# Kernel optimization log

Hardware: AMD Instinct MI355X
Metric: run time of the kernel (lower is better)

## Reference

```python
import jax, jax.numpy as jnp
import numpy as np

N, E, D, ED, H = 4096, 262144, 256, 64, 8
HD = D // H


def _ln(x, g, b, eps=1e-5):
    mu = jnp.mean(x, axis=-1, keepdims=True)
    var = jnp.mean((x - mu) ** 2, axis=-1, keepdims=True)
    return (x - mu) * jax.lax.rsqrt(var + eps) * g + b


def setup_inputs() -> dict:
    key = jax.random.key(0)
    ks = jax.random.split(key, 16)
    p = lambda k, s: (0.02 * jax.random.normal(k, s, dtype=jnp.float32))
    return {
        'x': jax.random.normal(ks[0], (N, D), dtype=jnp.float32),
        'edge_index': jax.random.randint(ks[1], (2, E), 0, N, dtype=jnp.int64),
        'edge_attr': jax.random.normal(ks[2], (E, ED), dtype=jnp.float32),
        'eps': jnp.zeros((), dtype=jnp.float32),  # GINEConv train_eps initial value 0
        'Wl': p(ks[3], (ED, D)), 'bl': jnp.zeros((D,), jnp.float32),
        'W1': p(ks[4], (D, D)), 'b1': jnp.zeros((D,), jnp.float32),
        'W2': p(ks[5], (D, D)), 'b2': jnp.zeros((D,), jnp.float32),
        'ln_l_g': jnp.ones((D,), jnp.float32), 'ln_l_b': jnp.zeros((D,), jnp.float32),
        'in_w': p(ks[6], (3 * D, D)), 'in_b': jnp.zeros((3 * D,), jnp.float32),
        'out_w': p(ks[7], (D, D)), 'out_b': jnp.zeros((D,), jnp.float32),
        'ln_a_g': jnp.ones((D,), jnp.float32), 'ln_a_b': jnp.zeros((D,), jnp.float32),
        'Wf1': p(ks[8], (D, 2 * D)), 'bf1': jnp.zeros((2 * D,), jnp.float32),
        'Wf2': p(ks[9], (2 * D, D)), 'bf2': jnp.zeros((D,), jnp.float32),
        'ln_f_g': jnp.ones((D,), jnp.float32), 'ln_f_b': jnp.zeros((D,), jnp.float32),
    }


def reference(x, edge_index, edge_attr, eps, Wl, bl, W1, b1, W2, b2,
              ln_l_g, ln_l_b, in_w, in_b, out_w, out_b, ln_a_g, ln_a_b,
              Wf1, bf1, Wf2, bf2, ln_f_g, ln_f_b):
    n = x.shape[0]
    src, dst = edge_index[0], edge_index[1]
    # --- GINEConv: msg = relu(x_j + lin(edge_attr)), sum-aggregate, MLP((1+eps)x + agg)
    msg = jax.nn.relu(x[src] + edge_attr @ Wl + bl)            # [E, D]
    agg = jax.ops.segment_sum(msg, dst, num_segments=n)        # [N, D]
    h = (1.0 + eps) * x + agg
    h = jax.nn.elu(h @ W1 + b1) @ W2 + b2                      # local_mlp
    x = x + jax.nn.elu(_ln(h, ln_l_g, ln_l_b))                 # local residual (dropout=eval)
    # --- MultiheadAttention (single batch of all nodes)
    qkv = x @ in_w.T + in_b                                    # [N, 3D]
    q, k, v = jnp.split(qkv, 3, axis=-1)
    q = q.reshape(n, H, HD)
    k = k.reshape(n, H, HD)
    v = v.reshape(n, H, HD)
    scores = jnp.einsum('qhd,khd->hqk', q, k) / jnp.sqrt(jnp.float32(HD))
    attn = jax.nn.softmax(scores, axis=-1)
    o = jnp.einsum('hqk,khd->qhd', attn, v).reshape(n, D)
    o = o @ out_w.T + out_b
    x = x + _ln(o, ln_a_g, ln_a_b)
    # --- FFN (exact GELU as in torch nn.GELU default)
    f = jax.nn.gelu(x @ Wf1 + bf1, approximate=False) @ Wf2 + bf2
    x = x + _ln(f, ln_f_g, ln_f_b)
    return x
```

## Files before the change

### kernel.cpp

```cpp
#include <hip/hip_runtime.h>
#include <cstddef>

#define D 256
#define H 8
#define HD 32
#define ED 64

typedef __attribute__((ext_vector_type(8))) short short8;
typedef __attribute__((ext_vector_type(4))) short short4v;
typedef __attribute__((ext_vector_type(4))) float floatx4;

__device__ inline short f2bf(float f) {
    unsigned u = __float_as_uint(f);
    unsigned r = (u + 0x7fffu + ((u >> 16) & 1u)) >> 16;
    return (short)r;
}

template<int ACT> __device__ inline float act_f(float v) {
    if (ACT == 1) return fmaxf(v, 0.f);
    if (ACT == 2) return v > 0.f ? v : expm1f(v);
    if (ACT == 3) return 0.5f * v * (1.f + erff(v * 0.70710678118654752f));
    return v;
}

__device__ inline float wave_sum(float v) {
#pragma unroll
    for (int off = 32; off > 0; off >>= 1) v += __shfl_xor(v, off, 64);
    return v;
}

__global__ void zero_kernel(int* __restrict__ p, int n) {
    int i = blockIdx.x * 256 + threadIdx.x;
    if (i < n) p[i] = 0;
}

__global__ void hist_kernel(const int* __restrict__ ei, int* __restrict__ cnt, int E) {
    int e = blockIdx.x * 256 + threadIdx.x;
    if (e < E) atomicAdd(&cnt[ei[E + e]], 1);
}

__global__ __launch_bounds__(1024) void scan_kernel(int* __restrict__ cnt,
                                                    int* __restrict__ offs) {
    __shared__ int s[1024];
    int tid = threadIdx.x;
    int4 c = *(int4*)&cnt[tid * 4];
    int sum = c.x + c.y + c.z + c.w;
    s[tid] = sum;
    __syncthreads();
    for (int off = 1; off < 1024; off <<= 1) {
        int v = (tid >= off) ? s[tid - off] : 0;
        __syncthreads();
        s[tid] += v;
        __syncthreads();
    }
    int ex = s[tid] - sum;
    int o1 = ex + c.x, o2 = o1 + c.y, o3 = o2 + c.z;
    offs[tid * 4] = ex; offs[tid * 4 + 1] = o1;
    offs[tid * 4 + 2] = o2; offs[tid * 4 + 3] = o3;
    cnt[tid * 4] = ex; cnt[tid * 4 + 1] = o1;
    cnt[tid * 4 + 2] = o2; cnt[tid * 4 + 3] = o3;
    if (tid == 1023) offs[4096] = s[1023];
}

__global__ void scatter_kernel(const int* __restrict__ ei, int* __restrict__ cursor,
                               int* __restrict__ perm, int* __restrict__ srcp,
                               int* __restrict__ dstp, int E) {
    int e = blockIdx.x * 256 + threadIdx.x;
    if (e < E) {
        int d = ei[E + e];
        int pos = atomicAdd(&cursor[d], 1);
        perm[pos] = e;
        srcp[pos] = ei[e];
        dstp[pos] = d;
    }
}

__global__ void wlT_kernel(const float* __restrict__ Wl, short* __restrict__ WlT) {
    int idx = blockIdx.x * 256 + threadIdx.x;
    int n = idx >> 6, k = idx & 63;
    WlT[idx] = f2bf(Wl[k * D + n]);
}

__global__ void convt_kernel(const float* __restrict__ in, short* __restrict__ o,
                             int K, int Nc) {
    int idx = blockIdx.x * 256 + threadIdx.x;
    if (idx < K * Nc) {
        int n = idx / K, k = idx - n * K;
        o[idx] = f2bf(in[k * Nc + n]);
    }
}
__global__ void conv_kernel(const float* __restrict__ in, short* __restrict__ o, int total) {
    int idx = blockIdx.x * 256 + threadIdx.x;
    if (idx < total) o[idx] = f2bf(in[idx]);
}

__global__ void init_h_kernel(const float* __restrict__ x, const float* __restrict__ eps,
                              float* __restrict__ h, int total) {
    int i = blockIdx.x * 256 + threadIdx.x;
    if (i < total) h[i] = (1.f + eps[0]) * x[i];
}

__global__ __launch_bounds__(256) void edge_fused_kernel(
        const float* __restrict__ ea, const short* __restrict__ WlT,
        const float* __restrict__ bl, const float* __restrict__ x,
        const int* __restrict__ perm, const int* __restrict__ srcp,
        const int* __restrict__ dstp, float* __restrict__ h) {
    __shared__ __align__(16) short ea_s[64 * 72];
    int tid = threadIdx.x;
    int wave = tid >> 6, lane = tid & 63;
    int mm = lane & 15, quad = lane >> 4;
    int e0 = blockIdx.x * 64;
    int myperm = perm[e0 + lane];
    int mysrc  = srcp[e0 + lane];
    int mydst  = dstp[e0 + lane];
#pragma unroll
    for (int p = 0; p < 4; p++) {
        int slot = tid + p * 256;
        int row = slot >> 4, c4 = slot & 15;
        int prow = __shfl(myperm, row);
        float4 v = *(const float4*)&ea[(size_t)prow * ED + c4 * 4];
        short4v s; s[0] = f2bf(v.x); s[1] = f2bf(v.y); s[2] = f2bf(v.z); s[3] = f2bf(v.w);
        *(short4v*)&ea_s[row * 72 + c4 * 4] = s;
    }
    __syncthreads();
    short8 af[4][2];
#pragma unroll
    for (int t = 0; t < 4; t++)
#pragma unroll
        for (int q2 = 0; q2 < 2; q2++)
            af[t][q2] = *(const short8*)&WlT[(wave * 64 + t * 16 + mm) * 64 + q2 * 32 + quad * 8];
    floatx4 acc[4][4];
#pragma unroll
    for (int et = 0; et < 4; et++)
#pragma unroll
        for (int t = 0; t < 4; t++) acc[et][t] = (floatx4){0.f, 0.f, 0.f, 0.f};
#pragma unroll
    for (int et = 0; et < 4; et++) {
        short8 bf0 = *(const short8*)&ea_s[(et * 16 + mm) * 72 + quad * 8];
        short8 bf1 = *(const short8*)&ea_s[(et * 16 + mm) * 72 + 32 + quad * 8];
#pragma unroll
        for (int t = 0; t < 4; t++) {
            acc[et][t] = __builtin_amdgcn_mfma_f32_16x16x32_bf16(af[t][0], bf0, acc[et][t], 0, 0, 0);
            acc[et][t] = __builtin_amdgcn_mfma_f32_16x16x32_bf16(af[t][1], bf1, acc[et][t], 0, 0, 0);
        }
    }
    float4 blv[4];
#pragma unroll
    for (int t = 0; t < 4; t++)
        blv[t] = *(const float4*)&bl[wave * 64 + t * 16 + quad * 4];
#pragma unroll
    for (int et = 0; et < 4; et++) {
        int srci = __shfl(mysrc, et * 16 + mm);
        const float* xrow = x + (size_t)srci * D + wave * 64 + quad * 4;
#pragma unroll
        for (int t = 0; t < 4; t++) {
            float4 xv = *(const float4*)(xrow + t * 16);
            acc[et][t][0] = fmaxf(acc[et][t][0] + blv[t].x + xv.x, 0.f);
            acc[et][t][1] = fmaxf(acc[et][t][1] + blv[t].y + xv.y, 0.f);
            acc[et][t][2] = fmaxf(acc[et][t][2] + blv[t].z + xv.z, 0.f);
            acc[et][t][3] = fmaxf(acc[et][t][3] + blv[t].w + xv.w, 0.f);
        }
    }
    int prevd = __shfl_up(mydst, 1);
    bool bnd = (lane == 0) || (mydst != prevd);
    unsigned long long bmask = __ballot(bnd);
    unsigned long long m = bmask;
    while (m) {
        int segstart = (int)__builtin_ctzll(m);
        m &= m - 1;
        int segend = m ? (int)__builtin_ctzll(m) : 64;
        int segdst = __shfl(mydst, segstart);
        bool in0 = (0 * 16 + mm >= segstart) & (0 * 16 + mm < segend);
        bool in1 = (1 * 16 + mm >= segstart) & (1 * 16 + mm < segend);
        bool in2 = (2 * 16 + mm >= segstart) & (2 * 16 + mm < segend);
        bool in3 = (3 * 16 + mm >= segstart) & (3 * 16 + mm < segend);
        float* hrow = h + (size_t)segdst * D + wave * 64;
#pragma unroll
        for (int t = 0; t < 4; t++) {
#pragma unroll
            for (int j = 0; j < 4; j++) {
                float v = (in0 ? acc[0][t][j] : 0.f) + (in1 ? acc[1][t][j] : 0.f)
                        + (in2 ? acc[2][t][j] : 0.f) + (in3 ? acc[3][t][j] : 0.f);
                v += __shfl_xor(v, 1);
                v += __shfl_xor(v, 2);
                v += __shfl_xor(v, 4);
                v += __shfl_xor(v, 8);
                if (mm == 0) atomicAdd(&hrow[t * 16 + quad * 4 + j], v);
            }
        }
    }
}

#define GSTR 40
template<int ACT>
__global__ __launch_bounds__(256) void gemm_bf16_kernel(
        const float* __restrict__ A, const short* __restrict__ Bt,
        const float* __restrict__ bias, float* __restrict__ C,
        int M, int K, int Nc) {
    __shared__ __align__(16) short As[64 * GSTR];
    __shared__ __align__(16) short Bs[64 * GSTR];
    int tid = threadIdx.x;
    int wave = tid >> 6, lane = tid & 63;
    int mm = lane & 15, quad = lane >> 4;
    int wm = wave >> 1, wn = wave & 1;
    int m0 = blockIdx.y * 64, n0 = blockIdx.x * 64;
    floatx4 acc[2][2];
#pragma unroll
    for (int i = 0; i < 2; i++)
#pragma unroll
        for (int j = 0; j < 2; j++) acc[i][j] = (floatx4){0.f, 0.f, 0.f, 0.f};
    for (int k0 = 0; k0 < K; k0 += 32) {
#pragma unroll
        for (int p = 0; p < 2; p++) {
            int slot = tid + p * 256;
            int row = slot >> 3, c4 = slot & 7;
            float4 v = *(const float4*)&A[(size_t)(m0 + row) * K + k0 + c4 * 4];
            short4v s; s[0] = f2bf(v.x); s[1] = f2bf(v.y); s[2] = f2bf(v.z); s[3] = f2bf(v.w);
            *(short4v*)&As[row * GSTR + c4 * 4] = s;
        }
        {
            int row = tid >> 2, seg = tid & 3;
            short8 v = *(const short8*)&Bt[(size_t)(n0 + row) * K + k0 + seg * 8];
            *(short8*)&Bs[row * GSTR + seg * 8] = v;
        }
        __syncthreads();
        short8 af[2], bf[2];
#pragma unroll
        for (int t = 0; t < 2; t++) {
            af[t] = *(const short8*)&As[(wm * 32 + t * 16 + mm) * GSTR + quad * 8];
            bf[t] = *(const short8*)&Bs[(wn * 32 + t * 16 + mm) * GSTR + quad * 8];
        }
#pragma unroll
        for (int i = 0; i < 2; i++)
#pragma unroll
            for (int j = 0; j < 2; j++)
                acc[i][j] = __builtin_amdgcn_mfma_f32_16x16x32_bf16(af[i], bf[j], acc[i][j], 0, 0, 0);
        __syncthreads();
    }
#pragma unroll
    for (int i = 0; i < 2; i++) {
#pragma unroll
        for (int j = 0; j < 2; j++) {
            int ncol = n0 + wn * 32 + j * 16 + mm;
            float bv = bias[ncol];
#pragma unroll
            for (int r = 0; r < 4; r++) {
                int mrow = m0 + wm * 32 + i * 16 + quad * 4 + r;
                C[(size_t)mrow * Nc + ncol] = act_f<ACT>(acc[i][j][r] + bv);
            }
        }
    }
}

template<int ACT>
__global__ __launch_bounds__(256) void ln_res_kernel(
        const float* __restrict__ t, const float* __restrict__ res,
        const float* __restrict__ g, const float* __restrict__ b,
        float* __restrict__ out) {
    __shared__ float red[8];
    int row = blockIdx.x, tid = threadIdx.x;
    float v = t[(size_t)row * D + tid];
    int wid = tid >> 6, lane = tid & 63;
    float s = wave_sum(v);
    if (lane == 0) red[wid] = s;
    __syncthreads();
    float mu = (red[0] + red[1] + red[2] + red[3]) * (1.f / D);
    float dv = v - mu;
    float s2 = wave_sum(dv * dv);
    if (lane == 0) red[4 + wid] = s2;
    __syncthreads();
    float var = (red[4] + red[5] + red[6] + red[7]) * (1.f / D);
    float y = dv * rsqrtf(var + 1e-5f) * g[tid] + b[tid];
    y = act_f<ACT>(y);
    out[(size_t)row * D + tid] = res[(size_t)row * D + tid] + y;
}

#define KSTR 40
#define VSTR 136
#define ATILE 128
__global__ __launch_bounds__(256) void attn_mfma_kernel(
        const float* __restrict__ qkv, float* __restrict__ po,
        float* __restrict__ pm, float* __restrict__ pl, int N, int KC_) {
    __shared__ __align__(16) short Ks[ATILE * KSTR];
    __shared__ __align__(16) short VTs[HD * VSTR];
    const int tid = threadIdx.x;
    const int wave = tid >> 6, lane = tid & 63;
    const int mm = lane & 15, quad = lane >> 4;
    const int h = blockIdx.y, c = blockIdx.z;
    const int qbase = blockIdx.x * 64 + wave * 16;
    const float scale = 0.17677669529663687f;

    short8 qf;
    {
        const float* qrow = qkv + (size_t)(qbase + mm) * (3 * D) + h * HD + quad * 8;
        float4 a = *(const float4*)qrow;
        float4 b = *(const float4*)(qrow + 4);
        qf[0] = f2bf(a.x * scale); qf[1] = f2bf(a.y * scale);
        qf[2] = f2bf(a.z * scale); qf[3] = f2bf(a.w * scale);
        qf[4] = f2bf(b.x * scale); qf[5] = f2bf(b.y * scale);
        qf[6] = f2bf(b.z * scale); qf[7] = f2bf(b.w * scale);
    }
    floatx4 accA = {0.f, 0.f, 0.f, 0.f};
    floatx4 accB = {0.f, 0.f, 0.f, 0.f};
    float m_r = -1e30f, l_r = 0.f;

    const int kchunk = N / KC_;
    const int kstart = c * kchunk;
    const int krow0 = ((mm >> 2) << 3) | (mm & 3);

    for (int t0 = 0; t0 < kchunk; t0 += ATILE) {
#pragma unroll
        for (int p = 0; p < 4; p++) {
            int slot = tid + p * 256;
            int kr = slot >> 3, e4 = slot & 7;
            const float* krow = qkv + (size_t)(kstart + t0 + kr) * (3 * D) + D + h * HD + e4 * 4;
            float4 kv = *(const float4*)krow;
            short4v ks;
            ks[0] = f2bf(kv.x); ks[1] = f2bf(kv.y); ks[2] = f2bf(kv.z); ks[3] = f2bf(kv.w);
            *(short4v*)&Ks[kr * KSTR + e4 * 4] = ks;
            const float* vrow = qkv + (size_t)(kstart + t0 + kr) * (3 * D) + 2 * D + h * HD + e4 * 4;
            float4 vv = *(const float4*)vrow;
            VTs[(e4 * 4 + 0) * VSTR + kr] = f2bf(vv.x);
            VTs[(e4 * 4 + 1) * VSTR + kr] = f2bf(vv.y);
            VTs[(e4 * 4 + 2) * VSTR + kr] = f2bf(vv.z);
            VTs[(e4 * 4 + 3) * VSTR + kr] = f2bf(vv.w);
        }
        __syncthreads();
#pragma unroll
        for (int s = 0; s < ATILE / 32; s++) {
            int sb = s * 32;
            short8 kf0 = *(const short8*)&Ks[(sb + krow0) * KSTR + quad * 8];
            short8 kf1 = *(const short8*)&Ks[(sb + krow0 + 4) * KSTR + quad * 8];
            floatx4 zero = {0.f, 0.f, 0.f, 0.f};
            floatx4 s0 = __builtin_amdgcn_mfma_f32_16x16x32_bf16(kf0, qf, zero, 0, 0, 0);
            floatx4 s1 = __builtin_amdgcn_mfma_f32_16x16x32_bf16(kf1, qf, zero, 0, 0, 0);
            float mx = fmaxf(fmaxf(fmaxf(s0[0], s0[1]), fmaxf(s0[2], s0[3])),
                             fmaxf(fmaxf(s1[0], s1[1]), fmaxf(s1[2], s1[3])));
            mx = fmaxf(mx, __shfl_xor(mx, 16));
            mx = fmaxf(mx, __shfl_xor(mx, 32));
            float nm = fmaxf(m_r, mx);
            float alpha = __expf(m_r - nm);
            float p0[4], p1[4], ls = 0.f;
#pragma unroll
            for (int j = 0; j < 4; j++) {
                p0[j] = __expf(s0[j] - nm);
                p1[j] = __expf(s1[j] - nm);
                ls += p0[j] + p1[j];
            }
            ls += __shfl_xor(ls, 16);
            ls += __shfl_xor(ls, 32);
            l_r = l_r * alpha + ls;
            m_r = nm;
            short8 pf;
#pragma unroll
            for (int j = 0; j < 4; j++) { pf[j] = f2bf(p0[j]); pf[4 + j] = f2bf(p1[j]); }
#pragma unroll
            for (int j = 0; j < 4; j++) { accA[j] *= alpha; accB[j] *= alpha; }
            short8 vf0 = *(const short8*)&VTs[mm * VSTR + sb + quad * 8];
            short8 vf1 = *(const short8*)&VTs[(mm + 16) * VSTR + sb + quad * 8];
            accA = __builtin_amdgcn_mfma_f32_16x16x32_bf16(vf0, pf, accA, 0, 0, 0);
            accB = __builtin_amdgcn_mfma_f32_16x16x32_bf16(vf1, pf, accB, 0, 0, 0);
        }
        __syncthreads();
    }
    size_t NH = (size_t)N * H;
    int qi = qbase + mm;
    size_t nh = (size_t)qi * H + h;
    if (lane < 16) {
        pm[(size_t)c * NH + nh] = m_r;
        pl[(size_t)c * NH + nh] = l_r;
    }
    float* op = po + ((size_t)c * NH + nh) * HD;
#pragma unroll
    for (int j = 0; j < 4; j++) {
        op[quad * 4 + j] = accA[j];
        op[16 + quad * 4 + j] = accB[j];
    }
}

__global__ __launch_bounds__(256) void attn_combine_kernel(
        const float* __restrict__ po, const float* __restrict__ pm,
        const float* __restrict__ pl, float* __restrict__ obuf, int N, int KC_) {
    int idx = blockIdx.x * 256 + threadIdx.x;
    int d = idx & (HD - 1);
    int nh = idx >> 5;
    size_t NH = (size_t)N * H;
    float M = -1e30f;
    for (int cc = 0; cc < KC_; cc++) M = fmaxf(M, pm[(size_t)cc * NH + nh]);
    float l = 0.f, o = 0.f;
    for (int cc = 0; cc < KC_; cc++) {
        float a = __expf(pm[(size_t)cc * NH + nh] - M);
        l += a * pl[(size_t)cc * NH + nh];
        o += a * po[((size_t)cc * NH + nh) * HD + d];
    }
    int n = nh >> 3, h = nh & (H - 1);
    obuf[(size_t)n * D + h * HD + d] = o / l;
}

extern "C" void kernel_launch(void* const* d_in, const int* in_sizes, int n_in,
                              void* d_out, int out_size, void* d_ws, size_t ws_size,
                              hipStream_t stream) {
    const float* x    = (const float*)d_in[0];
    const int*   ei   = (const int*)d_in[1];
    const float* ea   = (const float*)d_in[2];
    const float* eps  = (const float*)d_in[3];
    const float* Wl   = (const float*)d_in[4];
    const float* bl   = (const float*)d_in[5];
    const float* W1   = (const float*)d_in[6];
    const float* b1   = (const float*)d_in[7];
    const float* W2   = (const float*)d_in[8];
    const float* b2   = (const float*)d_in[9];
    const float* lnlg = (const float*)d_in[10];
    const float* lnlb = (const float*)d_in[11];
    const float* in_w = (const float*)d_in[12];
    const float* in_b = (const float*)d_in[13];
    const float* outw = (const float*)d_in[14];
    const float* outb = (const float*)d_in[15];
    const float* lnag = (const float*)d_in[16];
    const float* lnab = (const float*)d_in[17];
    const float* Wf1  = (const float*)d_in[18];
    const float* bf1  = (const float*)d_in[19];
    const float* Wf2  = (const float*)d_in[20];
    const float* bf2  = (const float*)d_in[21];
    const float* lnfg = (const float*)d_in[22];
    const float* lnfb = (const float*)d_in[23];
    float* out = (float*)d_out;

    const int N = in_sizes[0] / D;
    const int E = in_sizes[1] / 2;
    const size_t NF = (size_t)N * D;
    const size_t NH = (size_t)N * H;

    const int KCsel = 4;
    size_t floatEnd = (4 + (size_t)KCsel) * NF + 2 * (size_t)KCsel * NH;
    size_t offB = (floatEnd * 4 + 15) & ~(size_t)15;
    size_t intCount = (size_t)N + 3 * (size_t)E + (size_t)(N + 1);
    size_t wltOff = (offB + intCount * 4 + 15) & ~(size_t)15;

    float* w = (float*)d_ws;
    float* x1   = w;
    float* qkv  = w + NF;
    float* h    = w + 4 * NF;
    float* t1   = w + 5 * NF;
    float* t2   = w + 6 * NF;
    float* po   = w + 4 * NF;
    float* pm   = w + (4 + (size_t)KCsel) * NF;
    float* pl   = pm + (size_t)KCsel * NH;
    float* obuf = w + NF;
    float* t3   = w + 2 * NF;
    float* x2   = w + 3 * NF;
    float* f1   = w + 4 * NF;
    float* f2   = w + 6 * NF;

    char* base = (char*)d_ws;
    int* ibase  = (int*)(base + offB);
    int* cnt    = ibase;
    int* perm   = ibase + N;
    int* srcp   = perm + E;
    int* dstp   = srcp + E;
    int* offs   = dstp + E;
    short* WlT    = (short*)(base + wltOff);
    short* W1bt   = WlT + 16384;
    short* W2bt   = W1bt + 65536;
    short* inwbt  = W2bt + 65536;
    short* outwbt = inwbt + 196608;
    short* Wf1bt  = outwbt + 65536;
    short* Wf2bt  = Wf1bt + 131072;

    wlT_kernel<<<64, 256, 0, stream>>>(Wl, WlT);
    convt_kernel<<<256, 256, 0, stream>>>(W1, W1bt, 256, 256);
    convt_kernel<<<256, 256, 0, stream>>>(W2, W2bt, 256, 256);
    conv_kernel<<<768, 256, 0, stream>>>(in_w, inwbt, 196608);
    conv_kernel<<<256, 256, 0, stream>>>(outw, outwbt, 65536);
    convt_kernel<<<512, 256, 0, stream>>>(Wf1, Wf1bt, 256, 512);
    convt_kernel<<<512, 256, 0, stream>>>(Wf2, Wf2bt, 512, 256);

    zero_kernel<<<(N + 255) / 256, 256, 0, stream>>>(cnt, N);
    hist_kernel<<<(E + 255) / 256, 256, 0, stream>>>(ei, cnt, E);
    scan_kernel<<<1, 1024, 0, stream>>>(cnt, offs);
    scatter_kernel<<<(E + 255) / 256, 256, 0, stream>>>(ei, cnt, perm, srcp, dstp, E);
    init_h_kernel<<<(int)(NF / 256), 256, 0, stream>>>(x, eps, h, (int)NF);
    edge_fused_kernel<<<E / 64, 256, 0, stream>>>(ea, WlT, bl, x, perm, srcp, dstp, h);
    gemm_bf16_kernel<2><<<dim3(D / 64, N / 64), 256, 0, stream>>>(h, W1bt, b1, t1, N, D, D);
    gemm_bf16_kernel<0><<<dim3(D / 64, N / 64), 256, 0, stream>>>(t1, W2bt, b2, t2, N, D, D);
    ln_res_kernel<2><<<N, 256, 0, stream>>>(t2, x, lnlg, lnlb, x1);
    gemm_bf16_kernel<0><<<dim3(3 * D / 64, N / 64), 256, 0, stream>>>(x1, inwbt, in_b, qkv, N, D, 3 * D);
    attn_mfma_kernel<<<dim3(N / 64, H, KCsel), 256, 0, stream>>>(qkv, po, pm, pl, N, KCsel);
    attn_combine_kernel<<<(int)(NF / 256), 256, 0, stream>>>(po, pm, pl, obuf, N, KCsel);
    gemm_bf16_kernel<0><<<dim3(D / 64, N / 64), 256, 0, stream>>>(obuf, outwbt, outb, t3, N, D, D);
    ln_res_kernel<0><<<N, 256, 0, stream>>>(t3, x1, lnag, lnab, x2);
    gemm_bf16_kernel<3><<<dim3(2 * D / 64, N / 64), 256, 0, stream>>>(x2, Wf1bt, bf1, f1, N, D, 2 * D);
    gemm_bf16_kernel<0><<<dim3(D / 64, N / 64), 256, 0, stream>>>(f1, Wf2bt, bf2, f2, N, 2 * D, D);
    ln_res_kernel<0><<<N, 256, 0, stream>>>(f2, x2, lnfg, lnfb, out);

    (void)n_in; (void)out_size; (void)ws_size;
}
```

Before: 455.8 us.

## Merge prep kernels and double-buffer edge tiles in fused edge kernel

```diff
diff --git a/kernel.cpp b/kernel.cpp
--- a/kernel.cpp
+++ b/kernel.cpp
@@ -5,6 +5,7 @@
 #define H 8
 #define HD 32
 #define ED 64
+#define TPB 4
 
 typedef __attribute__((ext_vector_type(8))) short short8;
 typedef __attribute__((ext_vector_type(4))) short short4v;
@@ -29,9 +30,34 @@
     return v;
 }
 
-__global__ void zero_kernel(int* __restrict__ p, int n) {
-    int i = blockIdx.x * 256 + threadIdx.x;
-    if (i < n) p[i] = 0;
+__global__ void prep_kernel(
+        const float* __restrict__ Wl, const float* __restrict__ W1,
+        const float* __restrict__ W2, const float* __restrict__ in_w,
+        const float* __restrict__ outw, const float* __restrict__ Wf1,
+        const float* __restrict__ Wf2, const float* __restrict__ x,
+        const float* __restrict__ eps,
+        short* __restrict__ WlT, short* __restrict__ W1bt, short* __restrict__ W2bt,
+        short* __restrict__ inwbt, short* __restrict__ outwbt,
+        short* __restrict__ Wf1bt, short* __restrict__ Wf2bt,
+        int* __restrict__ cnt, float* __restrict__ h, int N, int NF) {
+    int idx = blockIdx.x * 256 + threadIdx.x;
+    if (idx < 16384) { int n = idx >> 6, k = idx & 63; WlT[idx] = f2bf(Wl[k * 256 + n]); return; }
+    idx -= 16384;
+    if (idx < 65536) { int n = idx >> 8, k = idx & 255; W1bt[idx] = f2bf(W1[k * 256 + n]); return; }
+    idx -= 65536;
+    if (idx < 65536) { int n = idx >> 8, k = idx & 255; W2bt[idx] = f2bf(W2[k * 256 + n]); return; }
+    idx -= 65536;
+    if (idx < 196608) { inwbt[idx] = f2bf(in_w[idx]); return; }
+    idx -= 196608;
+    if (idx < 65536) { outwbt[idx] = f2bf(outw[idx]); return; }
+    idx -= 65536;
+    if (idx < 131072) { int n = idx >> 8, k = idx & 255; Wf1bt[idx] = f2bf(Wf1[k * 512 + n]); return; }
+    idx -= 131072;
+    if (idx < 131072) { int n = idx >> 9, k = idx & 511; Wf2bt[idx] = f2bf(Wf2[k * 256 + n]); return; }
+    idx -= 131072;
+    if (idx < N) { cnt[idx] = 0; return; }
+    idx -= N;
+    if (idx < NF) { h[idx] = (1.f + eps[0]) * x[idx]; }
 }
 
 __global__ void hist_kernel(const int* __restrict__ ei, int* __restrict__ cnt, int E) {
@@ -75,118 +101,132 @@
     }
 }
 
-__global__ void wlT_kernel(const float* __restrict__ Wl, short* __restrict__ WlT) {
-    int idx = blockIdx.x * 256 + threadIdx.x;
-    int n = idx >> 6, k = idx & 63;
-    WlT[idx] = f2bf(Wl[k * D + n]);
-}
-
-__global__ void convt_kernel(const float* __restrict__ in, short* __restrict__ o,
-                             int K, int Nc) {
-    int idx = blockIdx.x * 256 + threadIdx.x;
-    if (idx < K * Nc) {
-        int n = idx / K, k = idx - n * K;
-        o[idx] = f2bf(in[k * Nc + n]);
-    }
-}
-__global__ void conv_kernel(const float* __restrict__ in, short* __restrict__ o, int total) {
-    int idx = blockIdx.x * 256 + threadIdx.x;
-    if (idx < total) o[idx] = f2bf(in[idx]);
-}
-
-__global__ void init_h_kernel(const float* __restrict__ x, const float* __restrict__ eps,
-                              float* __restrict__ h, int total) {
-    int i = blockIdx.x * 256 + threadIdx.x;
-    if (i < total) h[i] = (1.f + eps[0]) * x[i];
-}
-
 __global__ __launch_bounds__(256) void edge_fused_kernel(
         const float* __restrict__ ea, const short* __restrict__ WlT,
         const float* __restrict__ bl, const float* __restrict__ x,
         const int* __restrict__ perm, const int* __restrict__ srcp,
         const int* __restrict__ dstp, float* __restrict__ h) {
-    __shared__ __align__(16) short ea_s[64 * 72];
+    __shared__ __align__(16) short ea_s[2][64 * 72];
     int tid = threadIdx.x;
     int wave = tid >> 6, lane = tid & 63;
     int mm = lane & 15, quad = lane >> 4;
-    int e0 = blockIdx.x * 64;
-    int myperm = perm[e0 + lane];
-    int mysrc  = srcp[e0 + lane];
-    int mydst  = dstp[e0 + lane];
-#pragma unroll
-    for (int p = 0; p < 4; p++) {
-        int slot = tid + p * 256;
-        int row = slot >> 4, c4 = slot & 15;
-        int prow = __shfl(myperm, row);
-        float4 v = *(const float4*)&ea[(size_t)prow * ED + c4 * 4];
-        short4v s; s[0] = f2bf(v.x); s[1] = f2bf(v.y); s[2] = f2bf(v.z); s[3] = f2bf(v.w);
-        *(short4v*)&ea_s[row * 72 + c4 * 4] = s;
-    }
-    __syncthreads();
+    int base_e = blockIdx.x * (64 * TPB);
+
+    int myperm[TPB], mysrc[TPB], mydst[TPB];
+#pragma unroll
+    for (int t = 0; t < TPB; t++) {
+        myperm[t] = perm[base_e + t * 64 + lane];
+        mysrc[t]  = srcp[base_e + t * 64 + lane];
+        mydst[t]  = dstp[base_e + t * 64 + lane];
+    }
     short8 af[4][2];
 #pragma unroll
     for (int t = 0; t < 4; t++)
 #pragma unroll
         for (int q2 = 0; q2 < 2; q2++)
             af[t][q2] = *(const short8*)&WlT[(wave * 64 + t * 16 + mm) * 64 + q2 * 32 + quad * 8];
-    floatx4 acc[4][4];
-#pragma unroll
-    for (int et = 0; et < 4; et++)
-#pragma unroll
-        for (int t = 0; t < 4; t++) acc[et][t] = (floatx4){0.f, 0.f, 0.f, 0.f};
-#pragma unroll
-    for (int et = 0; et < 4; et++) {
-        short8 bf0 = *(const short8*)&ea_s[(et * 16 + mm) * 72 + quad * 8];
-        short8 bf1 = *(const short8*)&ea_s[(et * 16 + mm) * 72 + 32 + quad * 8];
-#pragma unroll
-        for (int t = 0; t < 4; t++) {
-            acc[et][t] = __builtin_amdgcn_mfma_f32_16x16x32_bf16(af[t][0], bf0, acc[et][t], 0, 0, 0);
-            acc[et][t] = __builtin_amdgcn_mfma_f32_16x16x32_bf16(af[t][1], bf1, acc[et][t], 0, 0, 0);
-        }
-    }
     float4 blv[4];
 #pragma unroll
     for (int t = 0; t < 4; t++)
         blv[t] = *(const float4*)&bl[wave * 64 + t * 16 + quad * 4];
-#pragma unroll
-    for (int et = 0; et < 4; et++) {
-        int srci = __shfl(mysrc, et * 16 + mm);
-        const float* xrow = x + (size_t)srci * D + wave * 64 + quad * 4;
-#pragma unroll
-        for (int t = 0; t < 4; t++) {
-            float4 xv = *(const float4*)(xrow + t * 16);
-            acc[et][t][0] = fmaxf(acc[et][t][0] + blv[t].x + xv.x, 0.f);
-            acc[et][t][1] = fmaxf(acc[et][t][1] + blv[t].y + xv.y, 0.f);
-            acc[et][t][2] = fmaxf(acc[et][t][2] + blv[t].z + xv.z, 0.f);
-            acc[et][t][3] = fmaxf(acc[et][t][3] + blv[t].w + xv.w, 0.f);
-        }
-    }
-    int prevd = __shfl_up(mydst, 1);
-    bool bnd = (lane == 0) || (mydst != prevd);
-    unsigned long long bmask = __ballot(bnd);
-    unsigned long long m = bmask;
-    while (m) {
-        int segstart = (int)__builtin_ctzll(m);
-        m &= m - 1;
-        int segend = m ? (int)__builtin_ctzll(m) : 64;
-        int segdst = __shfl(mydst, segstart);
-        bool in0 = (0 * 16 + mm >= segstart) & (0 * 16 + mm < segend);
-        bool in1 = (1 * 16 + mm >= segstart) & (1 * 16 + mm < segend);
-        bool in2 = (2 * 16 + mm >= segstart) & (2 * 16 + mm < segend);
-        bool in3 = (3 * 16 + mm >= segstart) & (3 * 16 + mm < segend);
-        float* hrow = h + (size_t)segdst * D + wave * 64;
-#pragma unroll
-        for (int t = 0; t < 4; t++) {
-#pragma unroll
-            for (int j = 0; j < 4; j++) {
-                float v = (in0 ? acc[0][t][j] : 0.f) + (in1 ? acc[1][t][j] : 0.f)
-                        + (in2 ? acc[2][t][j] : 0.f) + (in3 ? acc[3][t][j] : 0.f);
-                v += __shfl_xor(v, 1);
-                v += __shfl_xor(v, 2);
-                v += __shfl_xor(v, 4);
-                v += __shfl_xor(v, 8);
-                if (mm == 0) atomicAdd(&hrow[t * 16 + quad * 4 + j], v);
-            }
+
+    {
+        float4 r[4];
+#pragma unroll
+        for (int p = 0; p < 4; p++) {
+            int slot = tid + p * 256;
+            int row = slot >> 4, c4 = slot & 15;
+            int prow = __shfl(myperm[0], row);
+            r[p] = *(const float4*)&ea[(size_t)prow * ED + c4 * 4];
+        }
+#pragma unroll
+        for (int p = 0; p < 4; p++) {
+            int slot = tid + p * 256;
+            int row = slot >> 4, c4 = slot & 15;
+            short4v s; s[0] = f2bf(r[p].x); s[1] = f2bf(r[p].y); s[2] = f2bf(r[p].z); s[3] = f2bf(r[p].w);
+            *(short4v*)&ea_s[0][row * 72 + c4 * 4] = s;
+        }
+    }
+    __syncthreads();
+
+#pragma unroll
+    for (int t = 0; t < TPB; t++) {
+        const int buf = t & 1;
+        float4 pre[4];
+        if (t + 1 < TPB) {
+#pragma unroll
+            for (int p = 0; p < 4; p++) {
+                int slot = tid + p * 256;
+                int row = slot >> 4, c4 = slot & 15;
+                int prow = __shfl(myperm[t + 1], row);
+                pre[p] = *(const float4*)&ea[(size_t)prow * ED + c4 * 4];
+            }
+        }
+        floatx4 acc[4][4];
+#pragma unroll
+        for (int et = 0; et < 4; et++)
+#pragma unroll
+            for (int tt = 0; tt < 4; tt++) acc[et][tt] = (floatx4){0.f, 0.f, 0.f, 0.f};
+#pragma unroll
+        for (int et = 0; et < 4; et++) {
+            short8 bf0 = *(const short8*)&ea_s[buf][(et * 16 + mm) * 72 + quad * 8];
+            short8 bf1 = *(const short8*)&ea_s[buf][(et * 16 + mm) * 72 + 32 + quad * 8];
+#pragma unroll
+            for (int tt = 0; tt < 4; tt++) {
+                acc[et][tt] = __builtin_amdgcn_mfma_f32_16x16x32_bf16(af[tt][0], bf0, acc[et][tt], 0, 0, 0);
+                acc[et][tt] = __builtin_amdgcn_mfma_f32_16x16x32_bf16(af[tt][1], bf1, acc[et][tt], 0, 0, 0);
+            }
+        }
+#pragma unroll
+        for (int et = 0; et < 4; et++) {
+            int srci = __shfl(mysrc[t], et * 16 + mm);
+            const float* xrow = x + (size_t)srci * D + wave * 64 + quad * 4;
+#pragma unroll
+            for (int tt = 0; tt < 4; tt++) {
+                float4 xv = *(const float4*)(xrow + tt * 16);
+                acc[et][tt][0] = fmaxf(acc[et][tt][0] + blv[tt].x + xv.x, 0.f);
+                acc[et][tt][1] = fmaxf(acc[et][tt][1] + blv[tt].y + xv.y, 0.f);
+                acc[et][tt][2] = fmaxf(acc[et][tt][2] + blv[tt].z + xv.z, 0.f);
+                acc[et][tt][3] = fmaxf(acc[et][tt][3] + blv[tt].w + xv.w, 0.f);
+            }
+        }
+        int prevd = __shfl_up(mydst[t], 1);
+        bool bnd = (lane == 0) || (mydst[t] != prevd);
+        unsigned long long m = __ballot(bnd);
+        while (m) {
+            int segstart = (int)__builtin_ctzll(m);
+            m &= m - 1;
+            int segend = m ? (int)__builtin_ctzll(m) : 64;
+            int segdst = __shfl(mydst[t], segstart);
+            bool in0 = (0 * 16 + mm >= segstart) & (0 * 16 + mm < segend);
+            bool in1 = (1 * 16 + mm >= segstart) & (1 * 16 + mm < segend);
+            bool in2 = (2 * 16 + mm >= segstart) & (2 * 16 + mm < segend);
+            bool in3 = (3 * 16 + mm >= segstart) & (3 * 16 + mm < segend);
+            float* hrow = h + (size_t)segdst * D + wave * 64;
+#pragma unroll
+            for (int tt = 0; tt < 4; tt++) {
+#pragma unroll
+                for (int j = 0; j < 4; j++) {
+                    float v = (in0 ? acc[0][tt][j] : 0.f) + (in1 ? acc[1][tt][j] : 0.f)
+                            + (in2 ? acc[2][tt][j] : 0.f) + (in3 ? acc[3][tt][j] : 0.f);
+                    v += __shfl_xor(v, 1);
+                    v += __shfl_xor(v, 2);
+                    v += __shfl_xor(v, 4);
+                    v += __shfl_xor(v, 8);
+                    if (mm == 0) atomicAdd(&hrow[tt * 16 + quad * 4 + j], v);
+                }
+            }
+        }
+        if (t + 1 < TPB) {
+#pragma unroll
+            for (int p = 0; p < 4; p++) {
+                int slot = tid + p * 256;
+                int row = slot >> 4, c4 = slot & 15;
+                short4v s; s[0] = f2bf(pre[p].x); s[1] = f2bf(pre[p].y);
+                s[2] = f2bf(pre[p].z); s[3] = f2bf(pre[p].w);
+                *(short4v*)&ea_s[1 - buf][row * 72 + c4 * 4] = s;
+            }
+            __syncthreads();
         }
     }
 }
@@ -467,20 +507,16 @@
     short* Wf1bt  = outwbt + 65536;
     short* Wf2bt  = Wf1bt + 131072;
 
-    wlT_kernel<<<64, 256, 0, stream>>>(Wl, WlT);
-    convt_kernel<<<256, 256, 0, stream>>>(W1, W1bt, 256, 256);
-    convt_kernel<<<256, 256, 0, stream>>>(W2, W2bt, 256, 256);
-    conv_kernel<<<768, 256, 0, stream>>>(in_w, inwbt, 196608);
-    conv_kernel<<<256, 256, 0, stream>>>(outw, outwbt, 65536);
-    convt_kernel<<<512, 256, 0, stream>>>(Wf1, Wf1bt, 256, 512);
-    convt_kernel<<<512, 256, 0, stream>>>(Wf2, Wf2bt, 512, 256);
-
-    zero_kernel<<<(N + 255) / 256, 256, 0, stream>>>(cnt, N);
+    {
+        int total = 671744 + N + (int)NF;
+        prep_kernel<<<(total + 255) / 256, 256, 0, stream>>>(
+            Wl, W1, W2, in_w, outw, Wf1, Wf2, x, eps,
+            WlT, W1bt, W2bt, inwbt, outwbt, Wf1bt, Wf2bt, cnt, h, N, (int)NF);
+    }
     hist_kernel<<<(E + 255) / 256, 256, 0, stream>>>(ei, cnt, E);
     scan_kernel<<<1, 1024, 0, stream>>>(cnt, offs);
     scatter_kernel<<<(E + 255) / 256, 256, 0, stream>>>(ei, cnt, perm, srcp, dstp, E);
-    init_h_kernel<<<(int)(NF / 256), 256, 0, stream>>>(x, eps, h, (int)NF);
-    edge_fused_kernel<<<E / 64, 256, 0, stream>>>(ea, WlT, bl, x, perm, srcp, dstp, h);
+    edge_fused_kernel<<<E / (64 * TPB), 256, 0, stream>>>(ea, WlT, bl, x, perm, srcp, dstp, h);
     gemm_bf16_kernel<2><<<dim3(D / 64, N / 64), 256, 0, stream>>>(h, W1bt, b1, t1, N, D, D);
     gemm_bf16_kernel<0><<<dim3(D / 64, N / 64), 256, 0, stream>>>(t1, W2bt, b2, t2, N, D, D);
     ln_res_kernel<2><<<N, 256, 0, stream>>>(t2, x, lnlg, lnlb, x1);
```

Measured after the change: 426.5 us. 6.4% less time.
